# Optimization experiments

Measured on AMD Instinct MI355X. Metric: run time of the kernel, lower is better.

The kernel has to match this reference:

```python
import jax, jax.numpy as jnp
import numpy as np

EPS = 1e-6


def conv1x1(x, w, b):
    # x: [n,c,h,w], w: [o,c], b: [o]
    return jnp.einsum('nchw,oc->nohw', x, w) + b[None, :, None, None]


def maxpool2(x):
    n, c, h, w = x.shape
    return x.reshape(n, c, h // 2, 2, w // 2, 2).max(axis=(3, 5))


def resize_bilinear_ac(img, oh, ow):
    # bilinear resize with align_corners=True, img: [n,c,h,w]
    n, c, h, w = img.shape
    ys = jnp.linspace(0.0, h - 1.0, oh)
    xs = jnp.linspace(0.0, w - 1.0, ow)
    y0 = jnp.floor(ys).astype(jnp.int32)
    y1 = jnp.minimum(y0 + 1, h - 1)
    wy = (ys - y0.astype(img.dtype))
    x0 = jnp.floor(xs).astype(jnp.int32)
    x1 = jnp.minimum(x0 + 1, w - 1)
    wx = (xs - x0.astype(img.dtype))
    rows = img[:, :, y0, :] * (1.0 - wy)[None, None, :, None] + img[:, :, y1, :] * wy[None, None, :, None]
    return rows[:, :, :, x0] * (1.0 - wx)[None, None, None, :] + rows[:, :, :, x1] * wx[None, None, None, :]


def setup_inputs() -> dict:
    key = jax.random.key(0)
    ks = jax.random.split(key, 8)
    n, c, h, w = 4, 128, 256, 256
    ch = c // 2
    x = jax.random.normal(ks[0], (n, c, h, w), dtype=jnp.float32)
    depth_map = jax.random.uniform(ks[1], (n, 1, h, w), dtype=jnp.float32)
    s = 0.05
    return {
        'x': x,
        'depth_map': depth_map,
        'w_theta': jax.random.normal(ks[2], (ch, c), dtype=jnp.float32) * s,
        'b_theta': jnp.zeros((ch,), dtype=jnp.float32),
        'w_phi': jax.random.normal(ks[3], (ch, c), dtype=jnp.float32) * s,
        'b_phi': jnp.zeros((ch,), dtype=jnp.float32),
        'w_g': jax.random.normal(ks[4], (ch, c), dtype=jnp.float32) * s,
        'b_g': jnp.zeros((ch,), dtype=jnp.float32),
        'w_down': jnp.full((c, 1, 4, 4), 1.0 / 16.0, dtype=jnp.float32),  # depthwise 4x4 stride-4
        'w_z': jax.random.normal(ks[5], (c, ch), dtype=jnp.float32) * s,
        'b_z': jnp.zeros((c,), dtype=jnp.float32),
    }


def reference(x, depth_map, w_theta, b_theta, w_phi, b_phi, w_g, b_g, w_down, w_z, b_z):
    n, c, h, w = x.shape
    ch = c // 2
    # depthwise stride-4 downsample
    x_down = jax.lax.conv_general_dilated(
        x, w_down, window_strides=(4, 4), padding='VALID',
        feature_group_count=c, dimension_numbers=('NCHW', 'OIHW', 'NCHW'))
    # g, phi get extra 2x2 maxpool -> M = (h/8)*(w/8); theta stays at N = (h/4)*(w/4)
    g = maxpool2(conv1x1(x_down, w_g, b_g)).reshape(n, ch, -1).transpose(0, 2, 1)      # [n, M, ch]
    theta = conv1x1(x_down, w_theta, b_theta).reshape(n, ch, -1).transpose(0, 2, 1)    # [n, N, ch]
    phi = maxpool2(conv1x1(x_down, w_phi, b_phi)).reshape(n, ch, -1)                    # [n, ch, M]
    Ra = jax.nn.softmax(jnp.einsum('nic,ncj->nij', theta, phi), axis=2)                 # [n, N, M]
    # depth affinity
    d1 = resize_bilinear_ac(depth_map, h // 4, w // 4).reshape(n, -1, 1)                # [n, N, 1]
    d2 = resize_bilinear_ac(depth_map, h // 8, w // 8).reshape(n, 1, -1)                # [n, 1, M]
    Rd = jax.nn.softmax(jnp.minimum(d1 / (d2 + EPS), d2 / (d1 + EPS)), axis=2)          # [n, N, M]
    S = jax.nn.softmax(Ra * Rd, axis=2)
    y = jnp.einsum('nij,njc->nic', S, g).transpose(0, 2, 1).reshape(n, ch, h // 4, w // 4)
    return x + resize_bilinear_ac(conv1x1(y, w_z, b_z), h, w)
```

## Files before the change

### kernel.cpp

```cpp
#include <hip/hip_runtime.h>

#define EPSF 1e-6f

__device__ __forceinline__ float wave_max(float v) {
    #pragma unroll
    for (int m = 32; m; m >>= 1) v = fmaxf(v, __shfl_xor(v, m, 64));
    return v;
}
__device__ __forceinline__ float wave_sum(float v) {
    #pragma unroll
    for (int m = 32; m; m >>= 1) v += __shfl_xor(v, m, 64);
    return v;
}
__device__ __forceinline__ float lane_bcast(float v, int src) {
    return __int_as_float(__builtin_amdgcn_readlane(__float_as_int(v), src));
}

__global__ void k_down(const float* __restrict__ x, const float* __restrict__ wd,
                       float* __restrict__ xd) {
    int idx = blockIdx.x * 256 + threadIdx.x;
    int ow = idx & 63;
    int oh = (idx >> 6) & 63;
    int c  = (idx >> 12) & 127;
    int n  = idx >> 19;
    const float* xp = x + ((((size_t)n * 128 + c) * 256 + oh * 4) * 256) + ow * 4;
    const float* w  = wd + c * 16;
    float acc = 0.f;
    #pragma unroll
    for (int r = 0; r < 4; ++r) {
        float4 v = *reinterpret_cast<const float4*>(xp + (size_t)r * 256);
        acc += w[r*4+0]*v.x + w[r*4+1]*v.y + w[r*4+2]*v.z + w[r*4+3]*v.w;
    }
    xd[idx] = acc;
}

__global__ void k_conv(const float* __restrict__ xd,
                       const float* __restrict__ w0, const float* __restrict__ b0,
                       const float* __restrict__ w1, const float* __restrict__ b1,
                       const float* __restrict__ w2, const float* __restrict__ b2,
                       float* __restrict__ theta, float* __restrict__ phi_u,
                       float* __restrict__ g_u) {
    __shared__ float wl[64 * 128];
    int which = blockIdx.z;
    const float* w = (which == 0) ? w0 : (which == 1) ? w1 : w2;
    const float* b = (which == 0) ? b0 : (which == 1) ? b1 : b2;
    float* out = (which == 0) ? theta : (which == 1) ? phi_u : g_u;
    for (int i = threadIdx.x; i < 64 * 128; i += 256) wl[i] = w[i];
    __syncthreads();
    int n = blockIdx.y;
    int p = blockIdx.x * 256 + threadIdx.x;
    const float* xp = xd + (size_t)n * 128 * 4096 + p;
    float acc[64];
    #pragma unroll
    for (int o = 0; o < 64; ++o) acc[o] = b[o];
    for (int c = 0; c < 128; ++c) {
        float xv = xp[(size_t)c * 4096];
        #pragma unroll
        for (int o = 0; o < 64; ++o) acc[o] = fmaf(wl[o * 128 + c], xv, acc[o]);
    }
    float* op = out + (size_t)n * 64 * 4096 + p;
    #pragma unroll
    for (int o = 0; o < 64; ++o) op[(size_t)o * 4096] = acc[o];
}

__global__ void k_pool(const float* __restrict__ phi_u, const float* __restrict__ g_u,
                       float* __restrict__ phi, float* __restrict__ g_t) {
    int idx = blockIdx.x * 256 + threadIdx.x;
    int q = idx & 1023;
    int o = (idx >> 10) & 63;
    int n = idx >> 16;
    int qh = q >> 5, qw = q & 31;
    const float* sel = (blockIdx.y == 0) ? phi_u : g_u;
    const float* sp = sel + (((size_t)n * 64 + o) * 4096) + (qh * 2) * 64 + qw * 2;
    float m = fmaxf(fmaxf(sp[0], sp[1]), fmaxf(sp[64], sp[65]));
    if (blockIdx.y == 0) phi[idx] = m;
    else g_t[((size_t)n * 1024 + q) * 64 + o] = m;
}

__global__ void k_d12(const float* __restrict__ depth, float* __restrict__ d1,
                      float* __restrict__ d2) {
    int idx = blockIdx.x * 256 + threadIdx.x;
    const int T1 = 4 * 4096;
    bool is1 = idx < T1;
    int e = is1 ? idx : idx - T1;
    if (!is1 && e >= 4 * 1024) return;
    int n, oh, ow;
    float fy, fx;
    if (is1) { n = e >> 12; oh = (e >> 6) & 63; ow = e & 63;
               fy = (oh * 255.f) / 63.f;  fx = (ow * 255.f) / 63.f; }
    else     { n = e >> 10; oh = (e >> 5) & 31; ow = e & 31;
               fy = (oh * 255.f) / 31.f;  fx = (ow * 255.f) / 31.f; }
    int y0 = (int)floorf(fy); int y1 = min(y0 + 1, 255);
    int x0 = (int)floorf(fx); int x1 = min(x0 + 1, 255);
    float wy = fy - (float)y0, wx = fx - (float)x0;
    const float* dp = depth + (size_t)n * 65536;
    float v00 = dp[y0 * 256 + x0], v01 = dp[y0 * 256 + x1];
    float v10 = dp[y1 * 256 + x0], v11 = dp[y1 * 256 + x1];
    float r0 = v00 * (1.f - wx) + v01 * wx;
    float r1 = v10 * (1.f - wx) + v11 * wx;
    float v  = r0 * (1.f - wy) + r1 * wy;
    if (is1) d1[e] = v; else d2[e] = v;
}

#define ROWS 16
#define RPW  4
#define CCH  8
__global__ __launch_bounds__(256, 3)
void k_attn(const float* __restrict__ theta, const float* __restrict__ phi,
            const float* __restrict__ g_t, const float* __restrict__ d1,
            const float* __restrict__ d2, float* __restrict__ y_t) {
    __shared__ float pbuf[CCH * 1024];
    __shared__ float thl[64 * ROWS];
    __shared__ float d2l[1024];

    int n = blockIdx.y;
    int row0 = blockIdx.x * ROWS;
    int tid = threadIdx.x;
    int lane = tid & 63;
    int wv = tid >> 6;

    for (int i = tid; i < ROWS * 64; i += 256) {
        int r = i & (ROWS - 1); int c = i >> 4;
        thl[c * ROWS + r] = theta[((size_t)n * 64 + c) * 4096 + row0 + r];
    }
    for (int i = tid; i < 1024; i += 256) d2l[i] = d2[n * 1024 + i];

    float acc[RPW][16];
    #pragma unroll
    for (int r = 0; r < RPW; ++r)
        #pragma unroll
        for (int k = 0; k < 16; ++k) acc[r][k] = 0.f;

    for (int cc = 0; cc < 64; cc += CCH) {
        __syncthreads();
        {
            const float4* src = reinterpret_cast<const float4*>(phi + ((size_t)n * 64 + cc) * 1024);
            float4* dst = reinterpret_cast<float4*>(pbuf);
            for (int i = tid; i < CCH * 256; i += 256) dst[i] = src[i];
        }
        __syncthreads();
        #pragma unroll
        for (int c = 0; c < CCH; ++c) {
            float ph[16];
            #pragma unroll
            for (int k = 0; k < 16; ++k) ph[k] = pbuf[c * 1024 + k * 64 + lane];
            #pragma unroll
            for (int r = 0; r < RPW; ++r) {
                float th = thl[(cc + c) * ROWS + wv * RPW + r];
                #pragma unroll
                for (int k = 0; k < 16; ++k) acc[r][k] = fmaf(th, ph[k], acc[r][k]);
            }
        }
    }

    float d2v[16], d2inv[16];
    #pragma unroll
    for (int k = 0; k < 16; ++k) {
        d2v[k] = d2l[k * 64 + lane];
        d2inv[k] = 1.f / (d2v[k] + EPSF);
    }
    float yscale[RPW];
    #pragma unroll
    for (int r = 0; r < RPW; ++r) {
        float m = -1e30f;
        #pragma unroll
        for (int k = 0; k < 16; ++k) m = fmaxf(m, acc[r][k]);
        m = wave_max(m);
        float sum = 0.f;
        #pragma unroll
        for (int k = 0; k < 16; ++k) { float e = __expf(acc[r][k] - m); acc[r][k] = e; sum += e; }
        sum = wave_sum(sum);
        float inv_ra = 1.f / sum;
        float d1v = d1[n * 4096 + row0 + wv * RPW + r];
        float inv1 = 1.f / (d1v + EPSF);
        float rdl[16];
        float dm = -1e30f;
        #pragma unroll
        for (int k = 0; k < 16; ++k) {
            float v = fminf(d1v * d2inv[k], d2v[k] * inv1);
            rdl[k] = v; dm = fmaxf(dm, v);
        }
        dm = wave_max(dm);
        float dsum = 0.f;
        #pragma unroll
        for (int k = 0; k < 16; ++k) { float e = __expf(rdl[k] - dm); rdl[k] = e; dsum += e; }
        dsum = wave_sum(dsum);
        float inv = inv_ra / dsum;
        float pm = -1e30f;
        #pragma unroll
        for (int k = 0; k < 16; ++k) { float p = acc[r][k] * rdl[k] * inv; acc[r][k] = p; pm = fmaxf(pm, p); }
        pm = wave_max(pm);
        float ss = 0.f;
        #pragma unroll
        for (int k = 0; k < 16; ++k) { float e = __expf(acc[r][k] - pm); acc[r][k] = e; ss += e; }
        ss = wave_sum(ss);
        yscale[r] = 1.f / ss;
    }

    const float* gp = g_t + (size_t)n * 1024 * 64 + lane;
    float yacc[RPW] = {0.f, 0.f, 0.f, 0.f};
    #pragma unroll
    for (int k = 0; k < 16; ++k) {
        #pragma unroll 4
        for (int jj = 0; jj < 64; ++jj) {
            float gv = gp[(size_t)(k * 64 + jj) * 64];
            #pragma unroll
            for (int r = 0; r < RPW; ++r)
                yacc[r] = fmaf(lane_bcast(acc[r][k], jj), gv, yacc[r]);
        }
    }
    #pragma unroll
    for (int r = 0; r < RPW; ++r)
        y_t[((size_t)n * 64 + lane) * 4096 + row0 + wv * RPW + r] = yacc[r] * yscale[r];
}

__global__ void k_z(const float* __restrict__ y_t, const float* __restrict__ w_z,
                    const float* __restrict__ b_z, float* __restrict__ z) {
    __shared__ float wl[64 * 64];
    int ohalf = blockIdx.z;
    for (int i = threadIdx.x; i < 64 * 64; i += 256)
        wl[i] = w_z[(size_t)(ohalf * 64) * 64 + i];
    __syncthreads();
    int n = blockIdx.y;
    int p = blockIdx.x * 256 + threadIdx.x;
    float acc[64];
    #pragma unroll
    for (int o = 0; o < 64; ++o) acc[o] = b_z[ohalf * 64 + o];
    const float* yp = y_t + (size_t)n * 64 * 4096 + p;
    for (int c = 0; c < 64; ++c) {
        float yv = yp[(size_t)c * 4096];
        #pragma unroll
        for (int o = 0; o < 64; ++o) acc[o] = fmaf(wl[o * 64 + c], yv, acc[o]);
    }
    float* zp = z + ((size_t)n * 128 + ohalf * 64) * 4096 + p;
    #pragma unroll
    for (int o = 0; o < 64; ++o) zp[(size_t)o * 4096] = acc[o];
}

__global__ void k_final(const float* __restrict__ x, const float* __restrict__ z,
                        float* __restrict__ out) {
    int idx = blockIdx.x * 256 + threadIdx.x;
    int j4 = idx & 63;
    int i  = (idx >> 6) & 255;
    int c  = (idx >> 14) & 127;
    int n  = idx >> 21;
    float fy = (i * 63.f) / 255.f;
    int y0 = (int)floorf(fy); int y1 = min(y0 + 1, 63);
    float wy = fy - (float)y0;
    const float* zp = z + ((size_t)n * 128 + c) * 4096;
    float4 xo = reinterpret_cast<const float4*>(x)[idx];
    float res[4];
    #pragma unroll
    for (int m = 0; m < 4; ++m) {
        int j = j4 * 4 + m;
        float fx = (j * 63.f) / 255.f;
        int x0 = (int)floorf(fx); int x1 = min(x0 + 1, 63);
        float wx = fx - (float)x0;
        float r0 = zp[y0 * 64 + x0] * (1.f - wx) + zp[y0 * 64 + x1] * wx;
        float r1 = zp[y1 * 64 + x0] * (1.f - wx) + zp[y1 * 64 + x1] * wx;
        res[m] = r0 * (1.f - wy) + r1 * wy;
    }
    float4 o;
    o.x = xo.x + res[0]; o.y = xo.y + res[1];
    o.z = xo.z + res[2]; o.w = xo.w + res[3];
    reinterpret_cast<float4*>(out)[idx] = o;
}

extern "C" void kernel_launch(void* const* d_in, const int* in_sizes, int n_in,
                              void* d_out, int out_size, void* d_ws, size_t ws_size,
                              hipStream_t stream) {
    const float* x       = (const float*)d_in[0];
    const float* depth   = (const float*)d_in[1];
    const float* w_theta = (const float*)d_in[2];
    const float* b_theta = (const float*)d_in[3];
    const float* w_phi   = (const float*)d_in[4];
    const float* b_phi   = (const float*)d_in[5];
    const float* w_g     = (const float*)d_in[6];
    const float* b_g     = (const float*)d_in[7];
    const float* w_down  = (const float*)d_in[8];
    const float* w_z     = (const float*)d_in[9];
    const float* b_z     = (const float*)d_in[10];
    float* out = (float*)d_out;

    float* ws = (float*)d_ws;
    float* xd    = ws;
    float* theta = xd    + 2097152;
    float* phi_u = theta + 1048576;
    float* g_u   = phi_u + 1048576;
    float* phi   = g_u   + 1048576;
    float* g_t   = phi   + 262144;
    float* d1    = g_t   + 262144;
    float* d2    = d1    + 16384;
    float* y_t   = d2    + 4096;
    float* z     = y_t   + 1048576;

    k_down <<<8192, 256, 0, stream>>>(x, w_down, xd);
    k_conv <<<dim3(16, 4, 3), 256, 0, stream>>>(xd, w_theta, b_theta, w_phi, b_phi,
                                                w_g, b_g, theta, phi_u, g_u);
    k_pool <<<dim3(1024, 2), 256, 0, stream>>>(phi_u, g_u, phi, g_t);
    k_d12  <<<80, 256, 0, stream>>>(depth, d1, d2);
    k_attn <<<dim3(256, 4), 256, 0, stream>>>(theta, phi, g_t, d1, d2, y_t);
    k_z    <<<dim3(16, 4, 2), 256, 0, stream>>>(y_t, w_z, b_z, z);
    k_final<<<32768, 256, 0, stream>>>(x, z, out);
}
```

Measured before the change: 769.4 us.

## Read conv weights via scalar loads, fuse depth softmax passes, raise attn occupancy

The 1x1 conv kernels no longer stage weights in LDS. Their weight reads are wave-uniform, so the compiler can use scalar loads, and the block-level sync goes away. In the attention kernel the depth-affinity softmax and the product with Ra are fused into one pass. The per-row max is computed before the inv scaling, which removes the d2v and rdl register arrays and one loop. The launch bound is raised to 4 blocks per SM, which risks register spills and recomputes the depth ratio twice.

```diff
diff --git a/kernel.cpp b/kernel.cpp
--- a/kernel.cpp
+++ b/kernel.cpp
@@ -40,13 +40,10 @@
                        const float* __restrict__ w2, const float* __restrict__ b2,
                        float* __restrict__ theta, float* __restrict__ phi_u,
                        float* __restrict__ g_u) {
-    __shared__ float wl[64 * 128];
     int which = blockIdx.z;
     const float* w = (which == 0) ? w0 : (which == 1) ? w1 : w2;
     const float* b = (which == 0) ? b0 : (which == 1) ? b1 : b2;
     float* out = (which == 0) ? theta : (which == 1) ? phi_u : g_u;
-    for (int i = threadIdx.x; i < 64 * 128; i += 256) wl[i] = w[i];
-    __syncthreads();
     int n = blockIdx.y;
     int p = blockIdx.x * 256 + threadIdx.x;
     const float* xp = xd + (size_t)n * 128 * 4096 + p;
@@ -56,7 +53,7 @@
     for (int c = 0; c < 128; ++c) {
         float xv = xp[(size_t)c * 4096];
         #pragma unroll
-        for (int o = 0; o < 64; ++o) acc[o] = fmaf(wl[o * 128 + c], xv, acc[o]);
+        for (int o = 0; o < 64; ++o) acc[o] = fmaf(w[o * 128 + c], xv, acc[o]);
     }
     float* op = out + (size_t)n * 64 * 4096 + p;
     #pragma unroll
@@ -105,7 +102,7 @@
 #define ROWS 16
 #define RPW  4
 #define CCH  8
-__global__ __launch_bounds__(256, 3)
+__global__ __launch_bounds__(256, 4)
 void k_attn(const float* __restrict__ theta, const float* __restrict__ phi,
             const float* __restrict__ g_t, const float* __restrict__ d1,
             const float* __restrict__ d2, float* __restrict__ y_t) {
@@ -153,12 +150,10 @@
         }
     }
 
-    float d2v[16], d2inv[16];
-    #pragma unroll
-    for (int k = 0; k < 16; ++k) {
-        d2v[k] = d2l[k * 64 + lane];
-        d2inv[k] = 1.f / (d2v[k] + EPSF);
-    }
+    float d2inv[16];
+    #pragma unroll
+    for (int k = 0; k < 16; ++k) d2inv[k] = 1.f / (d2l[k * 64 + lane] + EPSF);
+
     float yscale[RPW];
     #pragma unroll
     for (int r = 0; r < RPW; ++r) {
@@ -173,26 +168,33 @@
         float inv_ra = 1.f / sum;
         float d1v = d1[n * 4096 + row0 + wv * RPW + r];
         float inv1 = 1.f / (d1v + EPSF);
-        float rdl[16];
         float dm = -1e30f;
         #pragma unroll
         for (int k = 0; k < 16; ++k) {
-            float v = fminf(d1v * d2inv[k], d2v[k] * inv1);
-            rdl[k] = v; dm = fmaxf(dm, v);
+            float v = fminf(d1v * d2inv[k], d2l[k * 64 + lane] * inv1);
+            dm = fmaxf(dm, v);
         }
         dm = wave_max(dm);
-        float dsum = 0.f;
-        #pragma unroll
-        for (int k = 0; k < 16; ++k) { float e = __expf(rdl[k] - dm); rdl[k] = e; dsum += e; }
+        float dsum = 0.f, um = -1e30f;
+        #pragma unroll
+        for (int k = 0; k < 16; ++k) {
+            float v = fminf(d1v * d2inv[k], d2l[k * 64 + lane] * inv1);
+            float re = __expf(v - dm);
+            dsum += re;
+            float t = acc[r][k] * re;
+            acc[r][k] = t;
+            um = fmaxf(um, t);
+        }
         dsum = wave_sum(dsum);
+        um = wave_max(um);
         float inv = inv_ra / dsum;
-        float pm = -1e30f;
-        #pragma unroll
-        for (int k = 0; k < 16; ++k) { float p = acc[r][k] * rdl[k] * inv; acc[r][k] = p; pm = fmaxf(pm, p); }
-        pm = wave_max(pm);
+        float pm = um * inv;
         float ss = 0.f;
         #pragma unroll
-        for (int k = 0; k < 16; ++k) { float e = __expf(acc[r][k] - pm); acc[r][k] = e; ss += e; }
+        for (int k = 0; k < 16; ++k) {
+            float e = __expf(acc[r][k] * inv - pm);
+            acc[r][k] = e; ss += e;
+        }
         ss = wave_sum(ss);
         yscale[r] = 1.f / ss;
     }
@@ -216,21 +218,18 @@
 
 __global__ void k_z(const float* __restrict__ y_t, const float* __restrict__ w_z,
                     const float* __restrict__ b_z, float* __restrict__ z) {
-    __shared__ float wl[64 * 64];
     int ohalf = blockIdx.z;
-    for (int i = threadIdx.x; i < 64 * 64; i += 256)
-        wl[i] = w_z[(size_t)(ohalf * 64) * 64 + i];
-    __syncthreads();
     int n = blockIdx.y;
     int p = blockIdx.x * 256 + threadIdx.x;
     float acc[64];
     #pragma unroll
     for (int o = 0; o < 64; ++o) acc[o] = b_z[ohalf * 64 + o];
     const float* yp = y_t + (size_t)n * 64 * 4096 + p;
+    const float* w = w_z + (size_t)(ohalf * 64) * 64;
     for (int c = 0; c < 64; ++c) {
         float yv = yp[(size_t)c * 4096];
         #pragma unroll
-        for (int o = 0; o < 64; ++o) acc[o] = fmaf(wl[o * 64 + c], yv, acc[o]);
+        for (int o = 0; o < 64; ++o) acc[o] = fmaf(w[o * 64 + c], yv, acc[o]);
     }
     float* zp = z + ((size_t)n * 128 + ohalf * 64) * 4096 + p;
     #pragma unroll
```

Measured after the change: 702.1 us. -8.7%, faster.
